# Kernel tuning notes

Measured on AMD Instinct MI355X. Metric: run time of the kernel, lower is better.

The kernel has to match this reference:

```python
import jax, jax.numpy as jnp
import numpy as np

EMB = 1024
HEADS = 8
INNER = EMB // HEADS          # 128
HEAD_DIM = INNER // HEADS     # 16
SCALE = INNER ** -0.5         # note: module scales by inner_dim, not head_dim
EPS = 1e-5


def setup_inputs() -> dict:
    key = jax.random.key(0)
    ks = jax.random.split(key, 4)
    b, n = 16, 1024
    x = jax.random.normal(ks[0], (b, n, EMB), dtype=jnp.float32)
    gamma = jnp.ones((EMB,), dtype=jnp.float32)
    beta = jnp.zeros((EMB,), dtype=jnp.float32)
    w_qkv = jax.random.normal(ks[1], (EMB, 3 * INNER), dtype=jnp.float32) * (EMB ** -0.5)
    w_proj = jax.random.normal(ks[2], (INNER, EMB), dtype=jnp.float32) * (INNER ** -0.5)
    b_proj = jnp.zeros((EMB,), dtype=jnp.float32)
    return {"x": x, "gamma": gamma, "beta": beta, "w_qkv": w_qkv,
            "w_proj": w_proj, "b_proj": b_proj}


def reference(x, gamma, beta, w_qkv, w_proj, b_proj):
    b, n, _ = x.shape
    # LayerNorm
    mu = jnp.mean(x, axis=-1, keepdims=True)
    var = jnp.var(x, axis=-1, keepdims=True)
    xn = (x - mu) * jax.lax.rsqrt(var + EPS) * gamma + beta
    # QKV projection (bias=False): [b, n, 3*INNER]
    qkv = jnp.einsum('bne,ef->bnf', xn, w_qkv)
    q, k, v = jnp.split(qkv, 3, axis=-1)
    to_heads = lambda a: a.reshape(b, n, HEADS, HEAD_DIM).transpose(0, 2, 1, 3)
    q, k, v = to_heads(q) * SCALE, to_heads(k), to_heads(v)
    # full score matrix [b, h, n, n] (as the original einsum does)
    attn = jax.nn.softmax(jnp.einsum('bhid,bhjd->bhij', q, k), axis=-1)
    out = jnp.einsum('bhij,bhjd->bhid', attn, v)
    out = out.transpose(0, 2, 1, 3).reshape(b, n, INNER)
    return jnp.einsum('bni,ie->bne', out, w_proj) + b_proj
```

## Files before the change

kernel.cpp:

```cpp
#include <hip/hip_runtime.h>

#define LOG2E 1.44269504088896340736f
#define QSCALE (0.08838834764831845f * LOG2E)

using short8 = __attribute__((ext_vector_type(8))) short;
using f32x4  = __attribute__((ext_vector_type(4))) float;
using f32x16 = __attribute__((ext_vector_type(16))) float;

union U16B { uint4 u; short8 s; };

typedef __attribute__((address_space(3))) unsigned char lds_byte;
typedef const __attribute__((address_space(1))) unsigned char glb_byte;
#define GLOAD16(gp, lp) __builtin_amdgcn_global_load_lds((glb_byte*)(gp), (lds_byte*)(lp), 16, 0, 0)

static __device__ __forceinline__ unsigned short f2bf(float f){
  union { float f; unsigned int i; } c; c.f = f;
  unsigned int i = c.i;
  i += 0x7fffu + ((i >> 16) & 1u);
  return (unsigned short)(i >> 16);
}

__global__ __launch_bounds__(256) void k_ln(const float* __restrict__ x,
                                            const float* __restrict__ gamma,
                                            const float* __restrict__ beta,
                                            unsigned short* __restrict__ xn,
                                            const float* __restrict__ wqkv,
                                            const float* __restrict__ wproj,
                                            unsigned short* __restrict__ wqkvT,
                                            unsigned short* __restrict__ wprojT){
  if (blockIdx.x < 4096){
    const int tok = (blockIdx.x*256 + threadIdx.x) >> 6;
    const int l = threadIdx.x & 63;
    const float4* xr = (const float4*)(x + (size_t)tok*1024);
    float4 v[4];
    #pragma unroll
    for (int i=0;i<4;i++) v[i] = xr[l + i*64];
    float s = 0.f, s2 = 0.f;
    #pragma unroll
    for (int i=0;i<4;i++){
      s  += v[i].x+v[i].y+v[i].z+v[i].w;
      s2 += v[i].x*v[i].x+v[i].y*v[i].y+v[i].z*v[i].z+v[i].w*v[i].w;
    }
    #pragma unroll
    for (int o=32;o;o>>=1){ s += __shfl_xor(s,o); s2 += __shfl_xor(s2,o); }
    float mu   = s*(1.0f/1024.0f);
    float rstd = rsqrtf(s2*(1.0f/1024.0f) - mu*mu + 1e-5f);
    ushort4* xo = (ushort4*)(xn + (size_t)tok*1024);
    #pragma unroll
    for (int i=0;i<4;i++){
      float4 g = ((const float4*)gamma)[l + i*64];
      float4 b = ((const float4*)beta)[l + i*64];
      ushort4 o;
      o.x = f2bf((v[i].x-mu)*rstd*g.x + b.x);
      o.y = f2bf((v[i].y-mu)*rstd*g.y + b.y);
      o.z = f2bf((v[i].z-mu)*rstd*g.z + b.z);
      o.w = f2bf((v[i].w-mu)*rstd*g.w + b.w);
      xo[l + i*64] = o;
    }
  } else {
    int t = (blockIdx.x - 4096)*256 + threadIdx.x;
    if (t < 49152){
      int n = t>>7, k0 = (t&127)*8;
      float sc = (n < 128) ? QSCALE : 1.0f;
      const float* src = wqkv + (size_t)k0*384 + n;
      ushort4 lo, hi;
      lo.x = f2bf(src[0]*sc);    lo.y = f2bf(src[384]*sc);
      lo.z = f2bf(src[768]*sc);  lo.w = f2bf(src[1152]*sc);
      hi.x = f2bf(src[1536]*sc); hi.y = f2bf(src[1920]*sc);
      hi.z = f2bf(src[2304]*sc); hi.w = f2bf(src[2688]*sc);
      *(ushort4*)(wqkvT + (size_t)n*1024 + k0)     = lo;
      *(ushort4*)(wqkvT + (size_t)n*1024 + k0 + 4) = hi;
    } else {
      int t2 = t - 49152;
      int n = t2>>4, k0 = (t2&15)*8;
      const float* src = wproj + (size_t)k0*1024 + n;
      ushort4 lo, hi;
      lo.x = f2bf(src[0]);    lo.y = f2bf(src[1024]);
      lo.z = f2bf(src[2048]); lo.w = f2bf(src[3072]);
      hi.x = f2bf(src[4096]); hi.y = f2bf(src[5120]);
      hi.z = f2bf(src[6144]); hi.w = f2bf(src[7168]);
      *(ushort4*)(wprojT + (size_t)n*128 + k0)     = lo;
      *(ushort4*)(wprojT + (size_t)n*128 + k0 + 4) = hi;
    }
  }
}

__global__ __launch_bounds__(256) void k_qkv(const unsigned short* __restrict__ xn,
                                             const unsigned short* __restrict__ wT,
                                             unsigned short* __restrict__ q,
                                             unsigned short* __restrict__ kbuf,
                                             unsigned short* __restrict__ vT){
  __shared__ __align__(16) unsigned short sm[2][64*64 + 128*64];
  const int tid = threadIdx.x;
  const int w = tid>>6, l = tid&63;
  const int m0 = blockIdx.x*64;
  const int sec = blockIdx.y;
  const int nb = sec*128;
  const int wm = (w>>1)*32, wn = (w&1)*64;
  f32x4 acc[2][4] = {};

  auto stage = [&](int buf, int k0){
    unsigned short* sA = &sm[buf][0];
    unsigned short* sB = &sm[buf][4096];
    #pragma unroll
    for (int i=0;i<2;i++){
      int chunk = i*256 + tid;
      int row = chunk>>3;
      int ch = (tid&7) ^ (row&7);
      GLOAD16(xn + (size_t)(m0+row)*1024 + k0 + ch*8,
              (char*)sA + (i*256 + w*64)*16);
    }
    #pragma unroll
    for (int i=0;i<4;i++){
      int chunk = i*256 + tid;
      int row = chunk>>3;
      int ch = (tid&7) ^ (row&7);
      GLOAD16(wT + (size_t)(nb+row)*1024 + k0 + ch*8,
              (char*)sB + (i*256 + w*64)*16);
    }
  };

  stage(0, 0);
  for (int t=0; t<16; ++t){
    const int cur = t & 1;
    if (t < 15){
      stage(cur^1, (t+1)<<6);
      asm volatile("s_waitcnt vmcnt(6)" ::: "memory");
    } else {
      asm volatile("s_waitcnt vmcnt(0)" ::: "memory");
    }
    __builtin_amdgcn_s_barrier();
    const unsigned short* sA = &sm[cur][0];
    const unsigned short* sB = &sm[cur][4096];
    #pragma unroll
    for (int s=0; s<2; ++s){
      short8 af[2], bfr[4];
      #pragma unroll
      for (int i=0;i<2;i++){
        int row = wm + i*16 + (l&15);
        U16B ta; ta.u = *(const uint4*)((const char*)sA + row*128 + ((s*64 + (l>>4)*16) ^ ((row&7)<<4)));
        af[i] = ta.s;
      }
      #pragma unroll
      for (int j=0;j<4;j++){
        int col = wn + j*16 + (l&15);
        U16B tb; tb.u = *(const uint4*)((const char*)sB + col*128 + ((s*64 + (l>>4)*16) ^ ((col&7)<<4)));
        bfr[j] = tb.s;
      }
      #pragma unroll
      for (int i=0;i<2;i++)
        #pragma unroll
        for (int j=0;j<4;j++)
          acc[i][j] = __builtin_amdgcn_mfma_f32_16x16x32_bf16(af[i], bfr[j], acc[i][j], 0,0,0);
    }
    __builtin_amdgcn_s_barrier();
  }

  const int b  = m0 >> 10;
  const int n0 = m0 & 1023;
  unsigned short* ep = &sm[0][0];
  if (sec < 2){
    #pragma unroll
    for (int fm=0; fm<2; ++fm)
      #pragma unroll
      for (int fn=0; fn<4; ++fn){
        int colf = wn + fn*16 + (l&15);
        #pragma unroll
        for (int i=0;i<4;i++){
          int row = wm + fm*16 + (l>>4)*4 + i;
          *(unsigned short*)((char*)ep + row*256 + ((2*colf) ^ ((row&15)<<4))) = f2bf(acc[fm][fn][i]);
        }
      }
    __syncthreads();
    unsigned short* dst = (sec==0) ? q : kbuf;
    #pragma unroll
    for (int it=0; it<4; ++it){
      int chunk = it*256 + tid;
      int tokl = chunk>>4, cc = chunk&15;
      uint4 vv = *(const uint4*)((const char*)ep + tokl*256 + ((cc*16) ^ ((tokl&15)<<4)));
      int h = cc>>1, d0 = (cc&1)*8;
      *(uint4*)(dst + ((size_t)(b*8 + h)*1024 + n0 + tokl)*16 + d0) = vv;
    }
  } else {
    #pragma unroll
    for (int fm=0; fm<2; ++fm)
      #pragma unroll
      for (int fn=0; fn<4; ++fn){
        int colf = wn + fn*16 + (l&15);
        int r0 = wm + fm*16 + (l>>4)*4;
        ushort4 pk;
        pk.x = f2bf(acc[fm][fn][0]); pk.y = f2bf(acc[fm][fn][1]);
        pk.z = f2bf(acc[fm][fn][2]); pk.w = f2bf(acc[fm][fn][3]);
        *(ushort4*)((char*)ep + colf*128 + ((2*r0) ^ ((colf&7)<<4))) = pk;
      }
    __syncthreads();
    #pragma unroll
    for (int it=0; it<4; ++it){
      int chunk = it*256 + tid;
      int f = chunk>>3, cc = chunk&7;
      uint4 vv = *(const uint4*)((const char*)ep + f*128 + ((cc*16) ^ ((f&7)<<4)));
      int h = f>>4, d = f&15;
      unsigned short* dp = vT + ((size_t)(b*8 + h)*16 + d)*1024 + n0 + (cc>>1)*16 + (cc&1)*4;
      *(uint2*)dp       = make_uint2(vv.x, vv.y);
      *(uint2*)(dp + 8) = make_uint2(vv.z, vv.w);
    }
  }
}

__global__ __launch_bounds__(256) void k_attn(const unsigned short* __restrict__ q,
                                              const unsigned short* __restrict__ kbuf,
                                              const unsigned short* __restrict__ vT,
                                              unsigned short* __restrict__ aout){
  const int bh = blockIdx.x;
  const int qc = blockIdx.y;
  const int w = threadIdx.x>>6, l = threadIdx.x&63;
  const int l31 = l&31, hi = l>>5;
  const int h = bh & 7;
  const int qrow = qc*128 + w*32 + l31;
  U16B qf_u; qf_u.u = *(const uint4*)(q + ((size_t)bh*1024 + qrow)*16 + hi*8);
  const short8 qf = qf_u.s;
  const unsigned short* kptr = kbuf + (size_t)bh*1024*16 + (size_t)l31*16 + hi*8;
  const unsigned short* vptr = vT + (size_t)bh*16*1024 + (size_t)(l31 & 15)*1024 + hi*8;
  const bool vok = (l31 < 16);
  const unsigned int ob = ((l31==16)||(l31==20)) ? 0x3F803F80u : 0u;
  const uint4 cvu = make_uint4(ob, ob, ob, ob);
  f32x16 acc = {};
  const f32x16 zz = {};

  U16B kf; kf.u = *(const uint4*)kptr; kptr += 512;
  U16B kn; kn.u = *(const uint4*)kptr; kptr += 512;
  U16B v0, v1; v0.u = cvu; v1.u = cvu;
  if (vok){ v0.u = *(const uint4*)vptr; v1.u = *(const uint4*)(vptr + 16); }
  vptr += 32;
  f32x16 sv = __builtin_amdgcn_mfma_f32_32x32x16_bf16(kf.s, qf, zz, 0,0,0);

  for (int t=0; t<32; ++t){
    U16B knn; knn.u = *(const uint4*)kptr; kptr += 512;
    U16B v0n, v1n; v0n.u = cvu; v1n.u = cvu;
    if (vok){ v0n.u = *(const uint4*)vptr; v1n.u = *(const uint4*)(vptr + 16); }
    vptr += 32;
    f32x16 svn = __builtin_amdgcn_mfma_f32_32x32x16_bf16(kn.s, qf, zz, 0,0,0);
    unsigned int u[8];
    #pragma unroll
    for (int j=0;j<8;j++){
      float a = __builtin_amdgcn_exp2f(sv[2*j]);
      float b = __builtin_amdgcn_exp2f(sv[2*j+1]);
      asm("v_cvt_pk_bf16_f32 %0, %1, %2" : "=v"(u[j]) : "v"(a), "v"(b));
    }
    U16B p0, p1;
    p0.u.x = u[0]; p0.u.y = u[1]; p0.u.z = u[2]; p0.u.w = u[3];
    p1.u.x = u[4]; p1.u.y = u[5]; p1.u.z = u[6]; p1.u.w = u[7];
    __builtin_amdgcn_s_setprio(1);
    acc = __builtin_amdgcn_mfma_f32_32x32x16_bf16(v0.s, p0.s, acc, 0,0,0);
    acc = __builtin_amdgcn_mfma_f32_32x32x16_bf16(v1.s, p1.s, acc, 0,0,0);
    __builtin_amdgcn_s_setprio(0);
    sv = svn; kn = knn; v0 = v0n; v1 = v1n;
  }
  float inv = 1.0f/acc[8];
  const size_t tok = (size_t)(bh>>3)*1024 + qrow;
  ushort4 o;
  o.x = f2bf(acc[0]*inv); o.y = f2bf(acc[1]*inv); o.z = f2bf(acc[2]*inv); o.w = f2bf(acc[3]*inv);
  *(ushort4*)(aout + tok*128 + h*16 + hi*4) = o;
  o.x = f2bf(acc[4]*inv); o.y = f2bf(acc[5]*inv); o.z = f2bf(acc[6]*inv); o.w = f2bf(acc[7]*inv);
  *(ushort4*)(aout + tok*128 + h*16 + 8 + hi*4) = o;
}

__global__ __launch_bounds__(256) void k_proj(const unsigned short* __restrict__ aout,
                                              const unsigned short* __restrict__ wT,
                                              const float* __restrict__ bias,
                                              float* __restrict__ out){
  __shared__ __align__(16) unsigned short sA[128*128];
  __shared__ __align__(16) unsigned short sB[128*128];
  const int tid = threadIdx.x;
  const int w = tid>>6, l = tid&63;
  const int m0 = blockIdx.x*128, nb = blockIdx.y*128;
  #pragma unroll
  for (int i=0;i<8;i++){
    int chunk = i*256 + tid;
    int row = chunk>>4;
    int ch = (tid&15) ^ (row&15);
    GLOAD16(aout + (size_t)(m0+row)*128 + ch*8, (char*)sA + (i*256 + w*64)*16);
  }
  #pragma unroll
  for (int i=0;i<8;i++){
    int chunk = i*256 + tid;
    int row = chunk>>4;
    int ch = (tid&15) ^ (row&15);
    GLOAD16(wT + (size_t)(nb+row)*128 + ch*8, (char*)sB + (i*256 + w*64)*16);
  }
  __syncthreads();
  const int wm = (w>>1)*64, wn = (w&1)*64;
  f32x4 acc[4][4] = {};
  #pragma unroll
  for (int s=0; s<4; ++s){
    short8 af[4], bfr[4];
    #pragma unroll
    for (int i=0;i<4;i++){
      int row = wm + i*16 + (l&15);
      U16B ta; ta.u = *(const uint4*)((const char*)sA + row*256 + ((s*64 + (l>>4)*16) ^ ((row&15)<<4)));
      af[i] = ta.s;
      int col = wn + i*16 + (l&15);
      U16B tb; tb.u = *(const uint4*)((const char*)sB + col*256 + ((s*64 + (l>>4)*16) ^ ((col&15)<<4)));
      bfr[i] = tb.s;
    }
    #pragma unroll
    for (int i=0;i<4;i++)
      #pragma unroll
      for (int j=0;j<4;j++)
        acc[i][j] = __builtin_amdgcn_mfma_f32_16x16x32_bf16(af[i], bfr[j], acc[i][j], 0,0,0);
  }
  #pragma unroll
  for (int fn=0; fn<4; ++fn){
    int col = nb + wn + fn*16 + (l&15);
    float bv = bias[col];
    #pragma unroll
    for (int fm=0; fm<4; ++fm)
      #pragma unroll
      for (int i=0;i<4;i++)
        out[(size_t)(m0 + wm + fm*16 + (l>>4)*4 + i)*1024 + col] = acc[fm][fn][i] + bv;
  }
}

extern "C" void kernel_launch(void* const* d_in, const int* in_sizes, int n_in,
                              void* d_out, int out_size, void* d_ws, size_t ws_size,
                              hipStream_t stream){
  (void)in_sizes; (void)n_in; (void)out_size; (void)ws_size;
  const float* x     = (const float*)d_in[0];
  const float* gamma = (const float*)d_in[1];
  const float* beta  = (const float*)d_in[2];
  const float* wqkv  = (const float*)d_in[3];
  const float* wproj = (const float*)d_in[4];
  const float* bias  = (const float*)d_in[5];
  float* out = (float*)d_out;
  char* ws = (char*)d_ws;
  unsigned short* xn = (unsigned short*)ws;
  unsigned short* q  = (unsigned short*)(ws + 33554432);
  unsigned short* kb = (unsigned short*)(ws + 33554432 + 4194304);
  unsigned short* vT = (unsigned short*)(ws + 33554432 + 2*4194304);
  unsigned short* ao = (unsigned short*)(ws + 33554432 + 3*4194304);
  unsigned short* wqkvT = (unsigned short*)(ws + 33554432 + 4*4194304);
  unsigned short* wprojT = (unsigned short*)(ws + 33554432 + 4*4194304 + 786432);
  k_ln  <<<dim3(4352), dim3(256), 0, stream>>>(x, gamma, beta, xn, wqkv, wproj, wqkvT, wprojT);
  k_qkv <<<dim3(256,3), dim3(256), 0, stream>>>(xn, wqkvT, q, kb, vT);
  k_attn<<<dim3(128,8), dim3(256), 0, stream>>>(q, kb, vT, ao);
  k_proj<<<dim3(128,8), dim3(256), 0, stream>>>(ao, wprojT, bias, out);
}
```

Before: 89.88 us.

## Split attention key range across two waves per query tile and reduce through LDS

Each attention block now runs 512 threads, with two waves per 32-query tile that each handle half of the 1024 keys. Per-wave unnormalized numerators and row sums are combined through shared memory before normalization and store. This doubles the number of waves and halves the serial loop length per wave, aiming to hide the latency of the exp/MFMA chain. In exchange it adds an LDS reduction, a block barrier, and a redundant Q load per wave pair. The exact-split sum is valid because softmax here uses no running max.

```diff
diff --git a/kernel.cpp b/kernel.cpp
--- a/kernel.cpp
+++ b/kernel.cpp
@@ -207,20 +207,23 @@
   }
 }
 
-__global__ __launch_bounds__(256) void k_attn(const unsigned short* __restrict__ q,
-                                              const unsigned short* __restrict__ kbuf,
-                                              const unsigned short* __restrict__ vT,
-                                              unsigned short* __restrict__ aout){
+__global__ __launch_bounds__(512, 8) void k_attn(const unsigned short* __restrict__ q,
+                                                 const unsigned short* __restrict__ kbuf,
+                                                 const unsigned short* __restrict__ vT,
+                                                 unsigned short* __restrict__ aout){
+  __shared__ float red[8][64][9];
   const int bh = blockIdx.x;
   const int qc = blockIdx.y;
-  const int w = threadIdx.x>>6, l = threadIdx.x&63;
+  const int tid = threadIdx.x;
+  const int wv = tid>>6, l = tid&63;
+  const int qsub = wv>>1, sp = wv&1;
   const int l31 = l&31, hi = l>>5;
   const int h = bh & 7;
-  const int qrow = qc*128 + w*32 + l31;
+  const int qrow = qc*128 + qsub*32 + l31;
   U16B qf_u; qf_u.u = *(const uint4*)(q + ((size_t)bh*1024 + qrow)*16 + hi*8);
   const short8 qf = qf_u.s;
-  const unsigned short* kptr = kbuf + (size_t)bh*1024*16 + (size_t)l31*16 + hi*8;
-  const unsigned short* vptr = vT + (size_t)bh*16*1024 + (size_t)(l31 & 15)*1024 + hi*8;
+  const unsigned short* kptr = kbuf + (size_t)bh*16384 + sp*8192 + (size_t)l31*16 + hi*8;
+  const unsigned short* vptr = vT + (size_t)bh*16384 + (size_t)(l31 & 15)*1024 + sp*512 + hi*8;
   const bool vok = (l31 < 16);
   const unsigned int ob = ((l31==16)||(l31==20)) ? 0x3F803F80u : 0u;
   const uint4 cvu = make_uint4(ob, ob, ob, ob);
@@ -234,7 +237,7 @@
   vptr += 32;
   f32x16 sv = __builtin_amdgcn_mfma_f32_32x32x16_bf16(kf.s, qf, zz, 0,0,0);
 
-  for (int t=0; t<32; ++t){
+  for (int t=0; t<16; ++t){
     U16B knn; knn.u = *(const uint4*)kptr; kptr += 512;
     U16B v0n, v1n; v0n.u = cvu; v1n.u = cvu;
     if (vok){ v0n.u = *(const uint4*)vptr; v1n.u = *(const uint4*)(vptr + 16); }
@@ -256,13 +259,28 @@
     __builtin_amdgcn_s_setprio(0);
     sv = svn; kn = knn; v0 = v0n; v1 = v1n;
   }
-  float inv = 1.0f/acc[8];
-  const size_t tok = (size_t)(bh>>3)*1024 + qrow;
-  ushort4 o;
-  o.x = f2bf(acc[0]*inv); o.y = f2bf(acc[1]*inv); o.z = f2bf(acc[2]*inv); o.w = f2bf(acc[3]*inv);
-  *(ushort4*)(aout + tok*128 + h*16 + hi*4) = o;
-  o.x = f2bf(acc[4]*inv); o.y = f2bf(acc[5]*inv); o.z = f2bf(acc[6]*inv); o.w = f2bf(acc[7]*inv);
-  *(ushort4*)(aout + tok*128 + h*16 + 8 + hi*4) = o;
+  #pragma unroll
+  for (int j=0;j<8;j++) red[wv][l][j] = acc[j];
+  red[wv][l][8] = acc[8];
+  __syncthreads();
+  if (sp == 0){
+    float n0 = red[wv][l][0] + red[wv+1][l][0];
+    float n1 = red[wv][l][1] + red[wv+1][l][1];
+    float n2 = red[wv][l][2] + red[wv+1][l][2];
+    float n3 = red[wv][l][3] + red[wv+1][l][3];
+    float n4 = red[wv][l][4] + red[wv+1][l][4];
+    float n5 = red[wv][l][5] + red[wv+1][l][5];
+    float n6 = red[wv][l][6] + red[wv+1][l][6];
+    float n7 = red[wv][l][7] + red[wv+1][l][7];
+    float ss = red[wv][l][8] + red[wv+1][l][8];
+    float inv = 1.0f/ss;
+    const size_t tok = (size_t)(bh>>3)*1024 + qrow;
+    ushort4 o;
+    o.x = f2bf(n0*inv); o.y = f2bf(n1*inv); o.z = f2bf(n2*inv); o.w = f2bf(n3*inv);
+    *(ushort4*)(aout + tok*128 + h*16 + hi*4) = o;
+    o.x = f2bf(n4*inv); o.y = f2bf(n5*inv); o.z = f2bf(n6*inv); o.w = f2bf(n7*inv);
+    *(ushort4*)(aout + tok*128 + h*16 + 8 + hi*4) = o;
+  }
 }
 
 __global__ __launch_bounds__(256) void k_proj(const unsigned short* __restrict__ aout,
@@ -342,6 +360,6 @@
   unsigned short* wprojT = (unsigned short*)(ws + 33554432 + 4*4194304 + 786432);
   k_ln  <<<dim3(4352), dim3(256), 0, stream>>>(x, gamma, beta, xn, wqkv, wproj, wqkvT, wprojT);
   k_qkv <<<dim3(256,3), dim3(256), 0, stream>>>(xn, wqkvT, q, kb, vT);
-  k_attn<<<dim3(128,8), dim3(256), 0, stream>>>(q, kb, vT, ao);
+  k_attn<<<dim3(128,8), dim3(512), 0, stream>>>(q, kb, vT, ao);
   k_proj<<<dim3(128,8), dim3(256), 0, stream>>>(ao, wprojT, bias, out);
 }
```

New measurement: 182.0 us. 2.02x slower.

## Rewrite attention with 16x16x32 MFMA, split-KV across waves, LDS reduction

Applied to the files above, without the earlier changes.

The attention kernel moves from 32x32x16 MFMA tiles, which wasted half the lanes on padding for the 16-dim head and folded the row sum into a ones-column trick, to 16x16x32 MFMA with only 16 query rows per wave. The key sequence is split in half across wave pairs, and partial outputs and explicit softmax sums are combined through shared memory. The V-transpose store layout in the QKV kernel is permuted to match the new B-operand ordering. The grid grows fourfold, raising parallelism and cutting padded MFMA work, at the cost of zero-filled half-lane K/Q operands, a block sync and no prefetch pipelining.

```diff
diff --git a/kernel.cpp b/kernel.cpp
--- a/kernel.cpp
+++ b/kernel.cpp
@@ -5,7 +5,6 @@
 
 using short8 = __attribute__((ext_vector_type(8))) short;
 using f32x4  = __attribute__((ext_vector_type(4))) float;
-using f32x16 = __attribute__((ext_vector_type(16))) float;
 
 union U16B { uint4 u; short8 s; };
 
@@ -200,7 +199,8 @@
       int f = chunk>>3, cc = chunk&7;
       uint4 vv = *(const uint4*)((const char*)ep + f*128 + ((cc*16) ^ ((f&7)<<4)));
       int h = f>>4, d = f&15;
-      unsigned short* dp = vT + ((size_t)(b*8 + h)*16 + d)*1024 + n0 + (cc>>1)*16 + (cc&1)*4;
+      int pos1 = ((cc&1)<<4) | ((cc&2)<<1);
+      unsigned short* dp = vT + ((size_t)(b*8 + h)*16 + d)*1024 + n0 + (cc>>2)*32 + pos1;
       *(uint2*)dp       = make_uint2(vv.x, vv.y);
       *(uint2*)(dp + 8) = make_uint2(vv.z, vv.w);
     }
@@ -211,58 +211,70 @@
                                               const unsigned short* __restrict__ kbuf,
                                               const unsigned short* __restrict__ vT,
                                               unsigned short* __restrict__ aout){
+  __shared__ float red[4][64][5];
   const int bh = blockIdx.x;
   const int qc = blockIdx.y;
-  const int w = threadIdx.x>>6, l = threadIdx.x&63;
-  const int l31 = l&31, hi = l>>5;
+  const int tid = threadIdx.x;
+  const int wv = tid>>6, l = tid&63;
+  const int qsub = wv>>1, sp = wv&1;
+  const int g = l>>4, l15 = l&15;
   const int h = bh & 7;
-  const int qrow = qc*128 + w*32 + l31;
-  U16B qf_u; qf_u.u = *(const uint4*)(q + ((size_t)bh*1024 + qrow)*16 + hi*8);
-  const short8 qf = qf_u.s;
-  const unsigned short* kptr = kbuf + (size_t)bh*1024*16 + (size_t)l31*16 + hi*8;
-  const unsigned short* vptr = vT + (size_t)bh*16*1024 + (size_t)(l31 & 15)*1024 + hi*8;
-  const bool vok = (l31 < 16);
-  const unsigned int ob = ((l31==16)||(l31==20)) ? 0x3F803F80u : 0u;
-  const uint4 cvu = make_uint4(ob, ob, ob, ob);
-  f32x16 acc = {};
-  const f32x16 zz = {};
-
-  U16B kf; kf.u = *(const uint4*)kptr; kptr += 512;
-  U16B kn; kn.u = *(const uint4*)kptr; kptr += 512;
-  U16B v0, v1; v0.u = cvu; v1.u = cvu;
-  if (vok){ v0.u = *(const uint4*)vptr; v1.u = *(const uint4*)(vptr + 16); }
-  vptr += 32;
-  f32x16 sv = __builtin_amdgcn_mfma_f32_32x32x16_bf16(kf.s, qf, zz, 0,0,0);
-
-  for (int t=0; t<32; ++t){
-    U16B knn; knn.u = *(const uint4*)kptr; kptr += 512;
-    U16B v0n, v1n; v0n.u = cvu; v1n.u = cvu;
-    if (vok){ v0n.u = *(const uint4*)vptr; v1n.u = *(const uint4*)(vptr + 16); }
-    vptr += 32;
-    f32x16 svn = __builtin_amdgcn_mfma_f32_32x32x16_bf16(kn.s, qf, zz, 0,0,0);
-    unsigned int u[8];
-    #pragma unroll
-    for (int j=0;j<8;j++){
-      float a = __builtin_amdgcn_exp2f(sv[2*j]);
-      float b = __builtin_amdgcn_exp2f(sv[2*j+1]);
-      asm("v_cvt_pk_bf16_f32 %0, %1, %2" : "=v"(u[j]) : "v"(a), "v"(b));
-    }
-    U16B p0, p1;
-    p0.u.x = u[0]; p0.u.y = u[1]; p0.u.z = u[2]; p0.u.w = u[3];
-    p1.u.x = u[4]; p1.u.y = u[5]; p1.u.z = u[6]; p1.u.w = u[7];
-    __builtin_amdgcn_s_setprio(1);
-    acc = __builtin_amdgcn_mfma_f32_32x32x16_bf16(v0.s, p0.s, acc, 0,0,0);
-    acc = __builtin_amdgcn_mfma_f32_32x32x16_bf16(v1.s, p1.s, acc, 0,0,0);
-    __builtin_amdgcn_s_setprio(0);
-    sv = svn; kn = knn; v0 = v0n; v1 = v1n;
-  }
-  float inv = 1.0f/acc[8];
-  const size_t tok = (size_t)(bh>>3)*1024 + qrow;
-  ushort4 o;
-  o.x = f2bf(acc[0]*inv); o.y = f2bf(acc[1]*inv); o.z = f2bf(acc[2]*inv); o.w = f2bf(acc[3]*inv);
-  *(ushort4*)(aout + tok*128 + h*16 + hi*4) = o;
-  o.x = f2bf(acc[4]*inv); o.y = f2bf(acc[5]*inv); o.z = f2bf(acc[6]*inv); o.w = f2bf(acc[7]*inv);
-  *(ushort4*)(aout + tok*128 + h*16 + 8 + hi*4) = o;
+  const int qrow = qc*32 + qsub*16 + l15;
+  const bool lo32 = (l < 32);
+  short8 qf = {0,0,0,0,0,0,0,0};
+  if (lo32){ U16B t_; t_.u = *(const uint4*)(q + ((size_t)bh*1024 + qrow)*16 + g*8); qf = t_.s; }
+  const unsigned short* kbase = kbuf + (size_t)bh*16384 + sp*8192;
+  const unsigned short* vbase = vT + (size_t)bh*16384 + (size_t)l15*1024 + sp*512;
+  f32x4 acc = {};
+  float ssum = 0.0f;
+  const f32x4 zz = {};
+
+  for (int t=0; t<16; ++t){
+    short8 k0f = {0,0,0,0,0,0,0,0}, k1f = {0,0,0,0,0,0,0,0};
+    if (lo32){
+      U16B a_, b_;
+      a_.u = *(const uint4*)(kbase + (size_t)(t*32 + l15)*16 + g*8);
+      b_.u = *(const uint4*)(kbase + (size_t)(t*32 + 16 + l15)*16 + g*8);
+      k0f = a_.s; k1f = b_.s;
+    }
+    U16B vv; vv.u = *(const uint4*)(vbase + t*32 + g*8);
+    f32x4 sv0 = __builtin_amdgcn_mfma_f32_16x16x32_bf16(k0f, qf, zz, 0,0,0);
+    f32x4 sv1 = __builtin_amdgcn_mfma_f32_16x16x32_bf16(k1f, qf, zz, 0,0,0);
+    float e0 = __builtin_amdgcn_exp2f(sv0[0]);
+    float e1 = __builtin_amdgcn_exp2f(sv0[1]);
+    float e2 = __builtin_amdgcn_exp2f(sv0[2]);
+    float e3 = __builtin_amdgcn_exp2f(sv0[3]);
+    float e4 = __builtin_amdgcn_exp2f(sv1[0]);
+    float e5 = __builtin_amdgcn_exp2f(sv1[1]);
+    float e6 = __builtin_amdgcn_exp2f(sv1[2]);
+    float e7 = __builtin_amdgcn_exp2f(sv1[3]);
+    ssum += ((e0+e1)+(e2+e3)) + ((e4+e5)+(e6+e7));
+    unsigned int u0,u1,u2,u3;
+    asm("v_cvt_pk_bf16_f32 %0, %1, %2" : "=v"(u0) : "v"(e0), "v"(e1));
+    asm("v_cvt_pk_bf16_f32 %0, %1, %2" : "=v"(u1) : "v"(e2), "v"(e3));
+    asm("v_cvt_pk_bf16_f32 %0, %1, %2" : "=v"(u2) : "v"(e4), "v"(e5));
+    asm("v_cvt_pk_bf16_f32 %0, %1, %2" : "=v"(u3) : "v"(e6), "v"(e7));
+    U16B p; p.u.x = u0; p.u.y = u1; p.u.z = u2; p.u.w = u3;
+    acc = __builtin_amdgcn_mfma_f32_16x16x32_bf16(vv.s, p.s, acc, 0,0,0);
+  }
+  red[wv][l][0] = acc[0]; red[wv][l][1] = acc[1];
+  red[wv][l][2] = acc[2]; red[wv][l][3] = acc[3];
+  red[wv][l][4] = ssum;
+  __syncthreads();
+  if (sp == 0){
+    float n0 = acc[0] + red[wv+1][l][0];
+    float n1 = acc[1] + red[wv+1][l][1];
+    float n2 = acc[2] + red[wv+1][l][2];
+    float n3 = acc[3] + red[wv+1][l][3];
+    float ss = ssum   + red[wv+1][l][4];
+    ss += __shfl_xor(ss, 16);
+    ss += __shfl_xor(ss, 32);
+    float inv = 1.0f/ss;
+    const size_t tok = (size_t)(bh>>3)*1024 + qrow;
+    ushort4 o;
+    o.x = f2bf(n0*inv); o.y = f2bf(n1*inv); o.z = f2bf(n2*inv); o.w = f2bf(n3*inv);
+    *(ushort4*)(aout + tok*128 + h*16 + g*4) = o;
+  }
 }
 
 __global__ __launch_bounds__(256) void k_proj(const unsigned short* __restrict__ aout,
@@ -342,6 +354,6 @@
   unsigned short* wprojT = (unsigned short*)(ws + 33554432 + 4*4194304 + 786432);
   k_ln  <<<dim3(4352), dim3(256), 0, stream>>>(x, gamma, beta, xn, wqkv, wproj, wqkvT, wprojT);
   k_qkv <<<dim3(256,3), dim3(256), 0, stream>>>(xn, wqkvT, q, kb, vT);
-  k_attn<<<dim3(128,8), dim3(256), 0, stream>>>(q, kb, vT, ao);
+  k_attn<<<dim3(128,32), dim3(256), 0, stream>>>(q, kb, vT, ao);
   k_proj<<<dim3(128,8), dim3(256), 0, stream>>>(ao, wprojT, bias, out);
 }
```

Measured after the change: 109.1 us. +21.4%, slower.
